# Kernel tuning notes

Hardware: AMD Instinct MI355X
Metric: run time of the kernel (lower is better)

## Reference

```python
import jax, jax.numpy as jnp
import numpy as np

N, D_IN, D_H, D_ATT, C_CLUST, N_CLS = 10000, 1024, 512, 256, 10, 4


def setup_inputs() -> dict:
    key = jax.random.key(0)
    ks = jax.random.split(key, 20)
    s = 0.02
    return {
        "x": jax.random.normal(ks[0], (N, D_IN), dtype=jnp.float32),
        "cluster_id": jax.random.randint(ks[1], (N,), 0, C_CLUST, dtype=jnp.int64),
        # per-cluster phi: Linear(1024->512) + ReLU + Linear(512->512) + ReLU
        "W1": s * jax.random.normal(ks[2], (C_CLUST, D_IN, D_H), dtype=jnp.float32),
        "b1": jnp.zeros((C_CLUST, D_H), dtype=jnp.float32),
        "W2": s * jax.random.normal(ks[3], (C_CLUST, D_H, D_H), dtype=jnp.float32),
        "b2": jnp.zeros((C_CLUST, D_H), dtype=jnp.float32),
        # attention_net fc: Linear(512->512)+ReLU
        "Wfc": s * jax.random.normal(ks[4], (D_H, D_H), dtype=jnp.float32),
        "bfc": jnp.zeros((D_H,), dtype=jnp.float32),
        # Attn_Net_Gated
        "Wa": s * jax.random.normal(ks[5], (D_H, D_ATT), dtype=jnp.float32),
        "ba": jnp.zeros((D_ATT,), dtype=jnp.float32),
        "Wb": s * jax.random.normal(ks[6], (D_H, D_ATT), dtype=jnp.float32),
        "bb": jnp.zeros((D_ATT,), dtype=jnp.float32),
        "Wc": s * jax.random.normal(ks[7], (D_ATT, 1), dtype=jnp.float32),
        "bc": jnp.zeros((1,), dtype=jnp.float32),
        # rho: Linear(512->256)+ReLU
        "Wr": s * jax.random.normal(ks[8], (D_H, D_ATT), dtype=jnp.float32),
        "br": jnp.zeros((D_ATT,), dtype=jnp.float32),
        # classifier: Linear(256->4)
        "Wcls": s * jax.random.normal(ks[9], (D_ATT, N_CLS), dtype=jnp.float32),
        "bcls": jnp.zeros((N_CLS,), dtype=jnp.float32),
    }


def reference(x, cluster_id, W1, b1, W2, b2, Wfc, bfc, Wa, ba, Wb, bb, Wc, bc, Wr, br, Wcls, bcls):
    C = W1.shape[0]
    # dense dispatch: apply every cluster's phi, then masked-mean per cluster
    # (ReLU is per-point elementwise, so masked mean == mean over members)
    h1 = jax.nn.relu(jnp.einsum('nd,cdh->cnh', x, W1) + b1[:, None, :])   # [C,N,512]
    h2 = jax.nn.relu(jnp.einsum('cnh,chk->cnk', h1, W2) + b2[:, None, :]) # [C,N,512]
    mask = (cluster_id[None, :] == jnp.arange(C)[:, None]).astype(h2.dtype)  # [C,N]
    counts = jnp.maximum(mask.sum(axis=1), 1.0)                           # [C]
    pooled = jnp.einsum('cnk,cn->ck', h2, mask) / counts[:, None]         # [C,512]
    # attention_net: fc + gated attention
    h = jax.nn.relu(pooled @ Wfc + bfc)                                   # [C,512]
    gate = jnp.tanh(h @ Wa + ba) * jax.nn.sigmoid(h @ Wb + bb)            # [C,256]
    A = (gate @ Wc + bc)                                                  # [C,1]
    A = jax.nn.softmax(A.T, axis=1)                                       # [1,C]
    h_path = A @ h                                                        # [1,512]
    hr = jax.nn.relu(h_path @ Wr + br)                                    # [1,256]
    logits = (hr[0] @ Wcls + bcls)[None, :]                               # [1,4]
    Y_prob = jax.nn.softmax(logits, axis=1)
    Y_hat = jnp.argmax(logits, axis=1)[:, None]
    return logits, Y_prob, Y_hat
```

## Files before the change

kernel.cpp:

```cpp
#include <hip/hip_runtime.h>
#include <math.h>

#define DIN 1024
#define DH 512
#define DATT 256
#define CNUM 10
#define NCLS 4
#define NH 64
#define NSC 40

typedef __attribute__((ext_vector_type(8))) short bf16x8;
typedef __attribute__((ext_vector_type(4))) float f32x4;
typedef unsigned short ushort_t;
typedef unsigned int uint_t;

__device__ inline ushort_t f2bf(float f) {
    uint_t u = __float_as_uint(f);
    u += 0x7FFF + ((u >> 16) & 1);
    return (ushort_t)(u >> 16);
}

__device__ inline void gl_lds16(const void* g, void* l) {
    __builtin_amdgcn_global_load_lds(
        (const __attribute__((address_space(1))) unsigned int*)g,
        (__attribute__((address_space(3))) unsigned int*)l, 16, 0, 0);
}


__global__ __launch_bounds__(256) void k_hist(
    const int* __restrict__ cid, int n, const float* __restrict__ bc,
    int* __restrict__ counts_part, float* __restrict__ pooled,
    float* __restrict__ a_logit, int* __restrict__ scat_pos)
{
    int bid = blockIdx.x;
    int t = threadIdx.x;

    if (bid < NH) {
        __shared__ int h[CNUM];
        int lane = t & 63;
        if (t < CNUM) h[t] = 0;
        __syncthreads();
        for (int i = bid * 256 + t; i < n; i += NH * 256) {
            int c = cid[i];
            #pragma unroll
            for (int cc = 0; cc < CNUM; cc++) {
                unsigned long long mask = __ballot(c == cc);
                if (mask == 0ull) continue;
                if (lane == (__ffsll(mask) - 1)) atomicAdd(&h[cc], __popcll(mask));
            }
        }
        __syncthreads();
        if (t < CNUM) counts_part[bid * 16 + t] = h[t];
        return;
    }

    for (int i = t; i < CNUM * DH; i += 256) pooled[i] = 0.f;
    if (t < CNUM) a_logit[t] = bc[0];
    if (t < CNUM) scat_pos[t] = 0;
}


__global__ __launch_bounds__(256) void k_scat2(
    const int* __restrict__ cid, int n, const int* __restrict__ counts_part,
    const float* __restrict__ x, const float* __restrict__ W1, const float* __restrict__ W2,
    ushort_t* __restrict__ xb, ushort_t* __restrict__ W1t, ushort_t* __restrict__ W2t,
    int nxb, int nw,
    int* __restrict__ counts, int* __restrict__ offsets, int* __restrict__ tile_off,
    int* __restrict__ scat_pos, int* __restrict__ bucket)
{
    int bid = blockIdx.x;
    int t = threadIdx.x;

    if (bid < NSC) {
        __shared__ int cnts[CNUM], off[CNUM];
        if (t < CNUM) {
            int s = 0;
            #pragma unroll 8
            for (int b = 0; b < NH; b++) s += counts_part[b * 16 + t];
            cnts[t] = s;
        }
        __syncthreads();
        if (t == 0) {
            int a = 0;
            for (int c = 0; c < CNUM; c++) { off[c] = a; a += cnts[c]; }
            if (bid == 0) {
                int aa = 0, tt = 0;
                for (int c = 0; c < CNUM; c++) {
                    offsets[c] = aa; tile_off[c] = tt; counts[c] = cnts[c];
                    aa += cnts[c]; tt += (cnts[c] + 127) >> 7;
                }
                offsets[CNUM] = aa; tile_off[CNUM] = tt;
            }
        }
        __syncthreads();
        int lane = t & 63;
        for (int i = bid * 256 + t; i < n; i += NSC * 256) {
            int c = cid[i];
            #pragma unroll
            for (int cc = 0; cc < CNUM; cc++) {
                unsigned long long mask = __ballot(c == cc);
                if (mask == 0ull) continue;
                int leader = __ffsll(mask) - 1;
                int basep = 0;
                if (lane == leader) basep = atomicAdd(&scat_pos[cc], __popcll(mask));
                basep = __shfl(basep, leader, 64);
                if (c == cc) {
                    int rank = __popcll(mask & ((1ull << lane) - 1ull));
                    bucket[off[cc] + basep + rank] = i;
                }
            }
        }
        return;
    }
    bid -= NSC;

    if (bid < nxb) {
        int row = bid * 2 + (t >> 7);
        if (row >= n) return;
        int col = (t & 127) * 8;
        const float* src = x + (size_t)row * DIN + col;
        float4 v0 = *(const float4*)(src);
        float4 v1 = *(const float4*)(src + 4);
        ushort_t* dst = xb + (size_t)row * DIN + col;
        *(ushort4*)dst = make_ushort4(f2bf(v0.x), f2bf(v0.y), f2bf(v0.z), f2bf(v0.w));
        *(ushort4*)(dst + 4) = make_ushort4(f2bf(v1.x), f2bf(v1.y), f2bf(v1.z), f2bf(v1.w));
        return;
    }
    bid -= nxb;

    if (bid < nw) {
        __shared__ float tile[64][65];
        int z = bid >> 7;
        int kx = (bid & 127) >> 3;
        int ny = bid & 7;
        const float* src; ushort_t* dst; int K;
        if (z < CNUM) { K = DIN; src = W1 + (size_t)z * K * DH; dst = W1t + (size_t)z * DH * K; }
        else          { K = DH;  src = W2 + (size_t)(z - CNUM) * K * DH; dst = W2t + (size_t)(z - CNUM) * DH * K; }
        int k0 = kx * 64;
        if (k0 >= K) return;
        int n0 = ny * 64;
        int rr = t >> 4;
        int cc = (t & 15) * 4;
        #pragma unroll
        for (int i = 0; i < 4; i++) {
            int row = rr + 16 * i;
            float4 v = *(const float4*)(src + (size_t)(k0 + row) * DH + n0 + cc);
            tile[row][cc + 0] = v.x; tile[row][cc + 1] = v.y;
            tile[row][cc + 2] = v.z; tile[row][cc + 3] = v.w;
        }
        __syncthreads();
        #pragma unroll
        for (int i = 0; i < 4; i++) {
            int nrow = rr + 16 * i;
            ushort4 o = make_ushort4(f2bf(tile[cc + 0][nrow]), f2bf(tile[cc + 1][nrow]),
                                     f2bf(tile[cc + 2][nrow]), f2bf(tile[cc + 3][nrow]));
            *(ushort4*)(dst + (size_t)(n0 + nrow) * K + k0 + cc) = o;
        }
    }
}


__device__ inline void gemm_tile(
    const ushort_t* aSrc0, const ushort_t* aSrc1,
    const ushort_t* bSrc0, const ushort_t* bSrc1, int Kd,
    f32x4 acc[4][4], ushort_t As[128][32], ushort_t Bs[128][32])
{
    int t = threadIdx.x;
    int lane = t & 63;
    int w = t >> 6, wr = w >> 1, wc = w & 1;
    int m = lane & 15, quad = lane >> 4;

    int r0 = t >> 2;
    int kc = (t & 3) * 8;

    ushort_t* aDst0 = &As[r0][kc];
    ushort_t* aDst1 = &As[64 + r0][kc];
    ushort_t* bDst0 = &Bs[r0][kc];
    ushort_t* bDst1 = &Bs[64 + r0][kc];

    const ushort_t* aF = &As[64 * wr + m][quad * 8];
    const ushort_t* bF = &Bs[64 * wc + m][quad * 8];

    for (int k0 = 0; k0 < Kd; k0 += 32) {
        __syncthreads();
        gl_lds16(aSrc0 + k0, aDst0);
        gl_lds16(aSrc1 + k0, aDst1);
        gl_lds16(bSrc0 + k0, bDst0);
        gl_lds16(bSrc1 + k0, bDst1);
        __syncthreads();
        bf16x8 a[4], b[4];
        #pragma unroll
        for (int mf = 0; mf < 4; mf++) a[mf] = *(const bf16x8*)(aF + mf * 16 * 32);
        #pragma unroll
        for (int nf = 0; nf < 4; nf++) b[nf] = *(const bf16x8*)(bF + nf * 16 * 32);
        #pragma unroll
        for (int mf = 0; mf < 4; mf++)
            #pragma unroll
            for (int nf = 0; nf < 4; nf++)
                acc[mf][nf] = __builtin_amdgcn_mfma_f32_16x16x32_bf16(a[mf], b[nf], acc[mf][nf], 0, 0, 0);
    }
}

__global__ __launch_bounds__(256, 1) void k_mfma1(
    const ushort_t* __restrict__ xb, const ushort_t* __restrict__ W1t,
    const float* __restrict__ b1, const int* __restrict__ bucket,
    const int* __restrict__ offsets, const int* __restrict__ counts,
    const int* __restrict__ tile_off,
    ushort_t* __restrict__ H1)
{
    __shared__ ushort_t As[128][32];
    __shared__ ushort_t Bs[128][32];
    int tx = blockIdx.y;
    if (tx >= tile_off[CNUM]) return;
    int c = 0;
    while (tx >= tile_off[c + 1]) c++;
    int m0 = (tx - tile_off[c]) * 128;
    int base = offsets[c], cnt = counts[c];
    int tile_n = blockIdx.x * 128;

    int t = threadIdx.x;
    int r0 = t >> 2;
    int kc = (t & 3) * 8;
    int ra0 = m0 + r0;      if (ra0 > cnt - 1) ra0 = cnt - 1; if (ra0 < 0) ra0 = 0;
    int ra1 = m0 + 64 + r0; if (ra1 > cnt - 1) ra1 = cnt - 1; if (ra1 < 0) ra1 = 0;
    const ushort_t* aSrc0 = xb + (size_t)bucket[base + ra0] * DIN + kc;
    const ushort_t* aSrc1 = xb + (size_t)bucket[base + ra1] * DIN + kc;
    const ushort_t* bSrc0 = W1t + ((size_t)c * DH + tile_n + r0) * DIN + kc;
    const ushort_t* bSrc1 = W1t + ((size_t)c * DH + tile_n + 64 + r0) * DIN + kc;

    f32x4 acc[4][4] = {};
    gemm_tile(aSrc0, aSrc1, bSrc0, bSrc1, DIN, acc, As, Bs);

    int lane = t & 63;
    int w = t >> 6, wr = w >> 1, wc = w & 1;
    int m = lane & 15, quad = lane >> 4;
    int col0 = tile_n + 64 * wc;
    #pragma unroll
    for (int nf = 0; nf < 4; nf++) {
        int col = col0 + 16 * nf + m;
        float bv = b1[c * DH + col];
        #pragma unroll
        for (int mf = 0; mf < 4; mf++) {
            int rowb = m0 + 64 * wr + 16 * mf + quad * 4;
            #pragma unroll
            for (int r = 0; r < 4; r++) {
                int row = rowb + r;
                if (row < cnt)
                    H1[(size_t)(base + row) * DH + col] = f2bf(fmaxf(acc[mf][nf][r] + bv, 0.f));
            }
        }
    }
}

__global__ __launch_bounds__(256, 1) void k_mfma2(
    const ushort_t* __restrict__ H1, const ushort_t* __restrict__ W2t,
    const float* __restrict__ b2,
    const int* __restrict__ offsets, const int* __restrict__ counts,
    const int* __restrict__ tile_off,
    float* __restrict__ pooled)
{
    __shared__ ushort_t As[128][32];
    __shared__ ushort_t Bs[128][32];
    int tx = blockIdx.y;
    if (tx >= tile_off[CNUM]) return;
    int c = 0;
    while (tx >= tile_off[c + 1]) c++;
    int m0 = (tx - tile_off[c]) * 128;
    int base = offsets[c], cnt = counts[c];
    int tile_n = blockIdx.x * 128;

    int t = threadIdx.x;
    int r0 = t >> 2;
    int kc = (t & 3) * 8;
    int ra0 = m0 + r0;      if (ra0 > cnt - 1) ra0 = cnt - 1; if (ra0 < 0) ra0 = 0;
    int ra1 = m0 + 64 + r0; if (ra1 > cnt - 1) ra1 = cnt - 1; if (ra1 < 0) ra1 = 0;
    const ushort_t* aSrc0 = H1 + (size_t)(base + ra0) * DH + kc;
    const ushort_t* aSrc1 = H1 + (size_t)(base + ra1) * DH + kc;
    const ushort_t* bSrc0 = W2t + ((size_t)c * DH + tile_n + r0) * DH + kc;
    const ushort_t* bSrc1 = W2t + ((size_t)c * DH + tile_n + 64 + r0) * DH + kc;

    f32x4 acc[4][4] = {};
    gemm_tile(aSrc0, aSrc1, bSrc0, bSrc1, DH, acc, As, Bs);

    int lane = t & 63;
    int w = t >> 6, wr = w >> 1, wc = w & 1;
    int m = lane & 15, quad = lane >> 4;
    int col0 = tile_n + 64 * wc;
    #pragma unroll
    for (int nf = 0; nf < 4; nf++) {
        int col = col0 + 16 * nf + m;
        float bv = b2[c * DH + col];
        float s = 0.f;
        #pragma unroll
        for (int mf = 0; mf < 4; mf++) {
            int rowb = m0 + 64 * wr + 16 * mf + quad * 4;
            #pragma unroll
            for (int r = 0; r < 4; r++) {
                int row = rowb + r;
                if (row < cnt) s += fmaxf(acc[mf][nf][r] + bv, 0.f);
            }
        }
        s += __shfl_xor(s, 16);
        s += __shfl_xor(s, 32);
        if (quad == 0) atomicAdd(&pooled[c * DH + col], s);
    }
}


__global__ __launch_bounds__(256) void k_fc2(
    const float* __restrict__ pooled, const int* __restrict__ counts,
    const float* __restrict__ Wfc, const float* __restrict__ bfc,
    float* __restrict__ hfc)
{
    int c = blockIdx.x;
    int c0 = blockIdx.y * 64;
    __shared__ float ps[DH];
    __shared__ float red[4][64];
    int t = threadIdx.x;
    float cnt = fmaxf((float)counts[c], 1.f);
    ps[t] = pooled[c * DH + t] / cnt;
    ps[t + 256] = pooled[c * DH + t + 256] / cnt;
    __syncthreads();
    int col = c0 + (t & 63);
    int ks = t >> 6;
    float acc = 0.f;
    #pragma unroll 8
    for (int k = ks * 128; k < ks * 128 + 128; k++)
        acc = fmaf(ps[k], Wfc[(size_t)k * DH + col], acc);
    red[ks][t & 63] = acc;
    __syncthreads();
    if (t < 64) {
        float v = red[0][t] + red[1][t] + red[2][t] + red[3][t] + bfc[c0 + t];
        hfc[c * DH + c0 + t] = fmaxf(v, 0.f);
    }
}

__global__ __launch_bounds__(256) void k_gate2(
    const float* __restrict__ hfc,
    const float* __restrict__ Wa, const float* __restrict__ ba,
    const float* __restrict__ Wb, const float* __restrict__ bb,
    const float* __restrict__ Wc,
    float* __restrict__ a_logit)
{
    int c = blockIdx.x;
    int d0 = blockIdx.y * 64;
    __shared__ float hf[DH];
    __shared__ float ra[4][64], rb[4][64];
    int t = threadIdx.x;
    hf[t] = hfc[c * DH + t];
    hf[t + 256] = hfc[c * DH + t + 256];
    __syncthreads();
    int d = d0 + (t & 63);
    int ks = t >> 6;
    float ga = 0.f, gb = 0.f;
    #pragma unroll 8
    for (int k = ks * 128; k < ks * 128 + 128; k++) {
        float h = hf[k];
        ga = fmaf(h, Wa[(size_t)k * DATT + d], ga);
        gb = fmaf(h, Wb[(size_t)k * DATT + d], gb);
    }
    ra[ks][t & 63] = ga;
    rb[ks][t & 63] = gb;
    __syncthreads();
    if (t < 64) {
        float sa = ra[0][t] + ra[1][t] + ra[2][t] + ra[3][t] + ba[d0 + t];
        float sb = rb[0][t] + rb[1][t] + rb[2][t] + rb[3][t] + bb[d0 + t];
        float g = tanhf(sa) * (1.f / (1.f + expf(-sb)));
        float p = g * Wc[d0 + t];
        #pragma unroll
        for (int off = 32; off >= 1; off >>= 1) p += __shfl_down(p, off, 64);
        if (t == 0) atomicAdd(&a_logit[c], p);
    }
}

__global__ __launch_bounds__(1024) void k_final(
    const float* __restrict__ hfc, const float* __restrict__ a_logit,
    const float* __restrict__ Wr, const float* __restrict__ br,
    const float* __restrict__ Wcls, const float* __restrict__ bcls,
    float* __restrict__ out)
{
    int t = threadIdx.x;
    __shared__ float hp[DH];
    __shared__ float r1[4][DATT];
    __shared__ float hr[DATT];
    __shared__ float wred[4][NCLS];

    float al[CNUM];
    float m = -1e30f;
    #pragma unroll
    for (int c = 0; c < CNUM; c++) { al[c] = a_logit[c]; m = fmaxf(m, al[c]); }
    float s = 0.f;
    #pragma unroll
    for (int c = 0; c < CNUM; c++) { al[c] = expf(al[c] - m); s += al[c]; }
    float inv = 1.f / s;

    if (t < DH) {
        float v = 0.f;
        #pragma unroll
        for (int c = 0; c < CNUM; c++) v = fmaf(al[c] * inv, hfc[c * DH + t], v);
        hp[t] = v;
    }
    __syncthreads();

    int d = t & 255;
    int ks = t >> 8;
    float acc = 0.f;
    #pragma unroll 8
    for (int k = ks * 128; k < ks * 128 + 128; k++)
        acc = fmaf(hp[k], Wr[(size_t)k * DATT + d], acc);
    r1[ks][d] = acc;
    __syncthreads();
    if (t < DATT)
        hr[t] = fmaxf(r1[0][t] + r1[1][t] + r1[2][t] + r1[3][t] + br[t], 0.f);
    __syncthreads();

    if (t < 256) {
        float h = hr[t];
        #pragma unroll
        for (int cls = 0; cls < NCLS; cls++) {
            float p = h * Wcls[(size_t)t * NCLS + cls];
            #pragma unroll
            for (int off = 32; off >= 1; off >>= 1) p += __shfl_down(p, off, 64);
            if ((t & 63) == 0) wred[t >> 6][cls] = p;
        }
    }
    __syncthreads();
    if (t == 0) {
        float lg[NCLS];
        #pragma unroll
        for (int cls = 0; cls < NCLS; cls++)
            lg[cls] = bcls[cls] + wred[0][cls] + wred[1][cls] + wred[2][cls] + wred[3][cls];
        float mm = lg[0];
        #pragma unroll
        for (int i = 1; i < NCLS; i++) mm = fmaxf(mm, lg[i]);
        float ss = 0.f, pr[NCLS];
        #pragma unroll
        for (int i = 0; i < NCLS; i++) { pr[i] = expf(lg[i] - mm); ss += pr[i]; }
        int am = 0; float best = lg[0];
        #pragma unroll
        for (int i = 1; i < NCLS; i++) if (lg[i] > best) { best = lg[i]; am = i; }
        #pragma unroll
        for (int i = 0; i < NCLS; i++) out[i] = lg[i];
        #pragma unroll
        for (int i = 0; i < NCLS; i++) out[4 + i] = pr[i] / ss;
        out[8] = (float)am;
    }
}


#define MT 64
#define NT 128
#define KT 32

__global__ __launch_bounds__(256) void k_gemm1(
    const float* __restrict__ x, const float* __restrict__ W1, const float* __restrict__ b1,
    const int* __restrict__ bucket, const int* __restrict__ offsets, const int* __restrict__ counts,
    float* __restrict__ H1)
{
    int c = blockIdx.z;
    int cnt = counts[c];
    int m0 = blockIdx.x * MT;
    if (m0 >= cnt) return;
    int rows = min(MT, cnt - m0);
    int n0 = blockIdx.y * NT;
    int base = offsets[c];

    __shared__ float As[KT][MT + 4];
    __shared__ float Bs[KT][NT];

    int t = threadIdx.x;
    int tr = t >> 4;
    int tc = t & 15;
    int lr = t >> 2;
    int lk = (t & 3) * 8;
    const float* xrow = nullptr;
    if (lr < rows) xrow = x + (size_t)bucket[base + m0 + lr] * DIN;

    float acc[4][8];
    #pragma unroll
    for (int i = 0; i < 4; i++)
        #pragma unroll
        for (int j = 0; j < 8; j++) acc[i][j] = 0.f;

    const float* Wp = W1 + (size_t)c * DIN * DH + n0;

    for (int k0 = 0; k0 < DIN; k0 += KT) {
        __syncthreads();
        if (xrow) {
            float4 v0 = *(const float4*)(xrow + k0 + lk);
            float4 v1 = *(const float4*)(xrow + k0 + lk + 4);
            As[lk + 0][lr] = v0.x; As[lk + 1][lr] = v0.y;
            As[lk + 2][lr] = v0.z; As[lk + 3][lr] = v0.w;
            As[lk + 4][lr] = v1.x; As[lk + 5][lr] = v1.y;
            As[lk + 6][lr] = v1.z; As[lk + 7][lr] = v1.w;
        } else {
            #pragma unroll
            for (int i = 0; i < 8; i++) As[lk + i][lr] = 0.f;
        }
        #pragma unroll
        for (int i = 0; i < 4; i++) {
            int idx = i * 256 + t;
            int kk = idx >> 5;
            int cv = idx & 31;
            *(float4*)&Bs[kk][cv * 4] = *(const float4*)(Wp + (size_t)(k0 + kk) * DH + cv * 4);
        }
        __syncthreads();
        #pragma unroll
        for (int k = 0; k < KT; k++) {
            float4 av  = *(const float4*)&As[k][4 * tr];
            float4 bv0 = *(const float4*)&Bs[k][4 * tc];
            float4 bv1 = *(const float4*)&Bs[k][64 + 4 * tc];
            float a[4] = {av.x, av.y, av.z, av.w};
            float b[8] = {bv0.x, bv0.y, bv0.z, bv0.w, bv1.x, bv1.y, bv1.z, bv1.w};
            #pragma unroll
            for (int i = 0; i < 4; i++)
                #pragma unroll
                for (int j = 0; j < 8; j++)
                    acc[i][j] = fmaf(a[i], b[j], acc[i][j]);
        }
    }

    #pragma unroll
    for (int i = 0; i < 4; i++) {
        int r = 4 * tr + i;
        if (r < rows) {
            size_t grow = (size_t)(base + m0 + r) * DH;
            #pragma unroll
            for (int j = 0; j < 8; j++) {
                int cidx = (j < 4) ? (4 * tc + j) : (64 + 4 * tc + (j - 4));
                int col = n0 + cidx;
                float v = acc[i][j] + b1[c * DH + col];
                H1[grow + col] = fmaxf(v, 0.f);
            }
        }
    }
}

__global__ __launch_bounds__(256) void k_gemm2(
    const float* __restrict__ H1, const float* __restrict__ W2, const float* __restrict__ b2,
    const int* __restrict__ offsets, const int* __restrict__ counts,
    float* __restrict__ pooled)
{
    int c = blockIdx.z;
    int cnt = counts[c];
    int m0 = blockIdx.x * MT;
    if (m0 >= cnt) return;
    int rows = min(MT, cnt - m0);
    int n0 = blockIdx.y * NT;
    int base = offsets[c];

    __shared__ float As[KT][MT + 4];
    __shared__ float Bs[KT][NT];
    __shared__ float red[16][NT];

    int t = threadIdx.x;
    int tr = t >> 4;
    int tc = t & 15;
    int lr = t >> 2;
    int lk = (t & 3) * 8;
    const float* arow = (lr < rows) ? (H1 + (size_t)(base + m0 + lr) * DH) : nullptr;

    float acc[4][8];
    #pragma unroll
    for (int i = 0; i < 4; i++)
        #pragma unroll
        for (int j = 0; j < 8; j++) acc[i][j] = 0.f;

    const float* Wp = W2 + (size_t)c * DH * DH + n0;

    for (int k0 = 0; k0 < DH; k0 += KT) {
        __syncthreads();
        if (arow) {
            float4 v0 = *(const float4*)(arow + k0 + lk);
            float4 v1 = *(const float4*)(arow + k0 + lk + 4);
            As[lk + 0][lr] = v0.x; As[lk + 1][lr] = v0.y;
            As[lk + 2][lr] = v0.z; As[lk + 3][lr] = v0.w;
            As[lk + 4][lr] = v1.x; As[lk + 5][lr] = v1.y;
            As[lk + 6][lr] = v1.z; As[lk + 7][lr] = v1.w;
        } else {
            #pragma unroll
            for (int i = 0; i < 8; i++) As[lk + i][lr] = 0.f;
        }
        #pragma unroll
        for (int i = 0; i < 4; i++) {
            int idx = i * 256 + t;
            int kk = idx >> 5;
            int cv = idx & 31;
            *(float4*)&Bs[kk][cv * 4] = *(const float4*)(Wp + (size_t)(k0 + kk) * DH + cv * 4);
        }
        __syncthreads();
        #pragma unroll
        for (int k = 0; k < KT; k++) {
            float4 av  = *(const float4*)&As[k][4 * tr];
            float4 bv0 = *(const float4*)&Bs[k][4 * tc];
            float4 bv1 = *(const float4*)&Bs[k][64 + 4 * tc];
            float a[4] = {av.x, av.y, av.z, av.w};
            float b[8] = {bv0.x, bv0.y, bv0.z, bv0.w, bv1.x, bv1.y, bv1.z, bv1.w};
            #pragma unroll
            for (int i = 0; i < 4; i++)
                #pragma unroll
                for (int j = 0; j < 8; j++)
                    acc[i][j] = fmaf(a[i], b[j], acc[i][j]);
        }
    }

    __syncthreads();
    #pragma unroll
    for (int j = 0; j < 8; j++) {
        int cidx = (j < 4) ? (4 * tc + j) : (64 + 4 * tc + (j - 4));
        float bias = b2[c * DH + n0 + cidx];
        float s = 0.f;
        #pragma unroll
        for (int i = 0; i < 4; i++) {
            if (4 * tr + i < rows) s += fmaxf(acc[i][j] + bias, 0.f);
        }
        red[tr][cidx] = s;
    }
    __syncthreads();
    if (t < NT) {
        float s = 0.f;
        #pragma unroll
        for (int r = 0; r < 16; r++) s += red[r][t];
        atomicAdd(&pooled[c * DH + n0 + t], s);
    }
}


extern "C" void kernel_launch(void* const* d_in, const int* in_sizes, int n_in,
                              void* d_out, int out_size, void* d_ws, size_t ws_size,
                              hipStream_t stream) {
    (void)n_in; (void)out_size;
    const float* x    = (const float*)d_in[0];
    const int*   cid  = (const int*)d_in[1];
    const float* W1   = (const float*)d_in[2];
    const float* b1   = (const float*)d_in[3];
    const float* W2   = (const float*)d_in[4];
    const float* b2   = (const float*)d_in[5];
    const float* Wfc  = (const float*)d_in[6];
    const float* bfc  = (const float*)d_in[7];
    const float* Wa   = (const float*)d_in[8];
    const float* ba   = (const float*)d_in[9];
    const float* Wb   = (const float*)d_in[10];
    const float* bb   = (const float*)d_in[11];
    const float* Wc   = (const float*)d_in[12];
    const float* bc   = (const float*)d_in[13];
    const float* Wr   = (const float*)d_in[14];
    const float* br   = (const float*)d_in[15];
    const float* Wcls = (const float*)d_in[16];
    const float* bcls = (const float*)d_in[17];
    float* out = (float*)d_out;
    float* ws  = (float*)d_ws;

    int n = in_sizes[1];

    float* pooled     = ws + 0;
    int*   counts     = (int*)(ws + 5120);
    int*   offsets    = (int*)(ws + 5136);
    int*   tile_off   = (int*)(ws + 5152);
    float* a_logit    = ws + 5168;
    int*   scat_pos   = (int*)(ws + 5184);
    float* hfc        = ws + 5200;
    int*   counts_part= (int*)(ws + 10320);
    int*   bucket     = (int*)(ws + 11344);

    size_t big0 = (((size_t)(11344 + n) * 4) + 255) & ~(size_t)255;
    size_t w1t_bytes = (size_t)CNUM * DH * DIN * 2;
    size_t w2t_bytes = (size_t)CNUM * DH * DH * 2;
    size_t h1_bytes  = (size_t)n * DH * 2;
    size_t xb_bytes  = (size_t)n * DIN * 2;
    size_t need = big0 + w1t_bytes + w2t_bytes + h1_bytes + xb_bytes;

    ushort_t* W1t = (ushort_t*)((char*)d_ws + big0);
    ushort_t* W2t = (ushort_t*)((char*)d_ws + big0 + w1t_bytes);
    ushort_t* H1  = (ushort_t*)((char*)d_ws + big0 + w1t_bytes + w2t_bytes);
    ushort_t* xb  = (ushort_t*)((char*)d_ws + big0 + w1t_bytes + w2t_bytes + h1_bytes);

    int fast = (ws_size >= need) ? 1 : 0;
    int nxb = fast ? (n + 1) / 2 : 0;
    int nw  = fast ? 128 * 2 * CNUM : 0;

    k_hist<<<NH + 1, 256, 0, stream>>>(cid, n, bc, counts_part, pooled, a_logit, scat_pos);
    k_scat2<<<NSC + nxb + nw, 256, 0, stream>>>(
        cid, n, counts_part, x, W1, W2, xb, W1t, W2t, nxb, nw,
        counts, offsets, tile_off, scat_pos, bucket);

    if (fast) {
        int maxt = n / 128 + CNUM;
        k_mfma1<<<dim3(4, maxt), 256, 0, stream>>>(xb, W1t, b1, bucket, offsets, counts, tile_off, H1);
        k_mfma2<<<dim3(4, maxt), 256, 0, stream>>>(H1, W2t, b2, offsets, counts, tile_off, pooled);
    } else {
        float* H1f = ws + ((11344 + n + 31) & ~31);
        dim3 gg((n + MT - 1) / MT, DH / NT, CNUM);
        k_gemm1<<<gg, 256, 0, stream>>>(x, W1, b1, bucket, offsets, counts, H1f);
        k_gemm2<<<gg, 256, 0, stream>>>(H1f, W2, b2, offsets, counts, pooled);
    }

    k_fc2<<<dim3(CNUM, 8), 256, 0, stream>>>(pooled, counts, Wfc, bfc, hfc);
    k_gate2<<<dim3(CNUM, 4), 256, 0, stream>>>(hfc, Wa, ba, Wb, bb, Wc, a_logit);
    k_final<<<1, 1024, 0, stream>>>(hfc, a_logit, Wr, br, Wcls, bcls, out);
}
```

Baseline: 230.4 us.

## Drop histogram pass, use per-cluster buckets and double-buffered swizzled MFMA GEMMs

Removes the separate histogram kernel by giving each cluster a fixed bucket region of size n, so the scatter atomics alone produce the counts; pooled and scat_pos are zeroed with a memset. The MFMA GEMMs move to K=64 tiles with double-buffered LDS, XOR-swizzled layout, explicit waitcnt and barrier scheduling, and an XCD-aware flat tile ordering. This is meant to cut a kernel launch and a serial dependency and to overlap global-to-LDS loads with MFMA work. In exchange the bucket and H1 buffers grow to CNUM*n, which raises workspace size. The change also uses more LDS per block, which may lower occupancy.

```diff
diff --git a/kernel.cpp b/kernel.cpp
--- a/kernel.cpp
+++ b/kernel.cpp
@@ -27,72 +27,23 @@
 }
 
 
-__global__ __launch_bounds__(256) void k_hist(
+__global__ __launch_bounds__(256) void k_prep(
     const int* __restrict__ cid, int n, const float* __restrict__ bc,
-    int* __restrict__ counts_part, float* __restrict__ pooled,
-    float* __restrict__ a_logit, int* __restrict__ scat_pos)
-{
-    int bid = blockIdx.x;
-    int t = threadIdx.x;
-
-    if (bid < NH) {
-        __shared__ int h[CNUM];
-        int lane = t & 63;
-        if (t < CNUM) h[t] = 0;
-        __syncthreads();
-        for (int i = bid * 256 + t; i < n; i += NH * 256) {
-            int c = cid[i];
-            #pragma unroll
-            for (int cc = 0; cc < CNUM; cc++) {
-                unsigned long long mask = __ballot(c == cc);
-                if (mask == 0ull) continue;
-                if (lane == (__ffsll(mask) - 1)) atomicAdd(&h[cc], __popcll(mask));
-            }
-        }
-        __syncthreads();
-        if (t < CNUM) counts_part[bid * 16 + t] = h[t];
-        return;
-    }
-
-    for (int i = t; i < CNUM * DH; i += 256) pooled[i] = 0.f;
-    if (t < CNUM) a_logit[t] = bc[0];
-    if (t < CNUM) scat_pos[t] = 0;
-}
-
-
-__global__ __launch_bounds__(256) void k_scat2(
-    const int* __restrict__ cid, int n, const int* __restrict__ counts_part,
     const float* __restrict__ x, const float* __restrict__ W1, const float* __restrict__ W2,
     ushort_t* __restrict__ xb, ushort_t* __restrict__ W1t, ushort_t* __restrict__ W2t,
     int nxb, int nw,
-    int* __restrict__ counts, int* __restrict__ offsets, int* __restrict__ tile_off,
-    int* __restrict__ scat_pos, int* __restrict__ bucket)
+    float* __restrict__ a_logit, int* __restrict__ scat_pos, int* __restrict__ bucket)
 {
     int bid = blockIdx.x;
     int t = threadIdx.x;
 
+    if (bid == 0) {
+        if (t < CNUM) a_logit[t] = bc[0];
+        return;
+    }
+    bid -= 1;
+
     if (bid < NSC) {
-        __shared__ int cnts[CNUM], off[CNUM];
-        if (t < CNUM) {
-            int s = 0;
-            #pragma unroll 8
-            for (int b = 0; b < NH; b++) s += counts_part[b * 16 + t];
-            cnts[t] = s;
-        }
-        __syncthreads();
-        if (t == 0) {
-            int a = 0;
-            for (int c = 0; c < CNUM; c++) { off[c] = a; a += cnts[c]; }
-            if (bid == 0) {
-                int aa = 0, tt = 0;
-                for (int c = 0; c < CNUM; c++) {
-                    offsets[c] = aa; tile_off[c] = tt; counts[c] = cnts[c];
-                    aa += cnts[c]; tt += (cnts[c] + 127) >> 7;
-                }
-                offsets[CNUM] = aa; tile_off[CNUM] = tt;
-            }
-        }
-        __syncthreads();
         int lane = t & 63;
         for (int i = bid * 256 + t; i < n; i += NSC * 256) {
             int c = cid[i];
@@ -106,7 +57,7 @@
                 basep = __shfl(basep, leader, 64);
                 if (c == cc) {
                     int rank = __popcll(mask & ((1ull << lane) - 1ull));
-                    bucket[off[cc] + basep + rank] = i;
+                    bucket[cc * n + basep + rank] = i;
                 }
             }
         }
@@ -115,15 +66,16 @@
     bid -= NSC;
 
     if (bid < nxb) {
-        int row = bid * 2 + (t >> 7);
+        int row = bid * 4 + (t >> 6);
         if (row >= n) return;
-        int col = (t & 127) * 8;
+        int col = (t & 63) * 16;
         const float* src = x + (size_t)row * DIN + col;
-        float4 v0 = *(const float4*)(src);
-        float4 v1 = *(const float4*)(src + 4);
         ushort_t* dst = xb + (size_t)row * DIN + col;
-        *(ushort4*)dst = make_ushort4(f2bf(v0.x), f2bf(v0.y), f2bf(v0.z), f2bf(v0.w));
-        *(ushort4*)(dst + 4) = make_ushort4(f2bf(v1.x), f2bf(v1.y), f2bf(v1.z), f2bf(v1.w));
+        #pragma unroll
+        for (int j = 0; j < 4; j++) {
+            float4 v = *(const float4*)(src + 4 * j);
+            *(ushort4*)(dst + 4 * j) = make_ushort4(f2bf(v.x), f2bf(v.y), f2bf(v.z), f2bf(v.w));
+        }
         return;
     }
     bid -= nxb;
@@ -160,76 +112,132 @@
 }
 
 
-__device__ inline void gemm_tile(
-    const ushort_t* aSrc0, const ushort_t* aSrc1,
-    const ushort_t* bSrc0, const ushort_t* bSrc1, int Kd,
-    f32x4 acc[4][4], ushort_t As[128][32], ushort_t Bs[128][32])
+__device__ inline void stage8(
+    const ushort_t* a0, const ushort_t* a1, const ushort_t* a2, const ushort_t* a3,
+    const ushort_t* b0, const ushort_t* b1, const ushort_t* b2, const ushort_t* b3,
+    int ko, ushort_t* As, ushort_t* Bs, int t)
+{
+    gl_lds16(a0 + ko, As + 0 * 2048 + t * 8);
+    gl_lds16(a1 + ko, As + 1 * 2048 + t * 8);
+    gl_lds16(a2 + ko, As + 2 * 2048 + t * 8);
+    gl_lds16(a3 + ko, As + 3 * 2048 + t * 8);
+    gl_lds16(b0 + ko, Bs + 0 * 2048 + t * 8);
+    gl_lds16(b1 + ko, Bs + 1 * 2048 + t * 8);
+    gl_lds16(b2 + ko, Bs + 2 * 2048 + t * 8);
+    gl_lds16(b3 + ko, Bs + 3 * 2048 + t * 8);
+}
+
+__device__ inline void mfma_tile(const ushort_t* As, const ushort_t* Bs,
+                                 f32x4 (&acc)[4][4], int wr, int wc, int m, int quad)
+{
+    bf16x8 a[2][4], b[2][4];
+    #pragma unroll
+    for (int ks = 0; ks < 2; ks++) {
+        int chunk = ((ks * 4 + quad) ^ (m & 7)) * 8;
+        #pragma unroll
+        for (int mf = 0; mf < 4; mf++)
+            a[ks][mf] = *(const bf16x8*)(As + (64 * wr + 16 * mf + m) * 64 + chunk);
+        #pragma unroll
+        for (int nf = 0; nf < 4; nf++)
+            b[ks][nf] = *(const bf16x8*)(Bs + (64 * wc + 16 * nf + m) * 64 + chunk);
+    }
+    asm volatile("s_waitcnt lgkmcnt(0)" ::: "memory");
+    __builtin_amdgcn_sched_barrier(0);
+    __builtin_amdgcn_s_barrier();
+    __builtin_amdgcn_sched_barrier(0);
+    #pragma unroll
+    for (int ks = 0; ks < 2; ks++)
+        #pragma unroll
+        for (int mf = 0; mf < 4; mf++)
+            #pragma unroll
+            for (int nf = 0; nf < 4; nf++)
+                acc[mf][nf] = __builtin_amdgcn_mfma_f32_16x16x32_bf16(a[ks][mf], b[ks][nf], acc[mf][nf], 0, 0, 0);
+}
+
+__device__ inline void gemm_loop(
+    const ushort_t* a0, const ushort_t* a1, const ushort_t* a2, const ushort_t* a3,
+    const ushort_t* b0, const ushort_t* b1, const ushort_t* b2, const ushort_t* b3,
+    int KT, f32x4 (&acc)[4][4], ushort_t* As, ushort_t* Bs)
 {
     int t = threadIdx.x;
     int lane = t & 63;
     int w = t >> 6, wr = w >> 1, wc = w & 1;
     int m = lane & 15, quad = lane >> 4;
 
-    int r0 = t >> 2;
-    int kc = (t & 3) * 8;
-
-    ushort_t* aDst0 = &As[r0][kc];
-    ushort_t* aDst1 = &As[64 + r0][kc];
-    ushort_t* bDst0 = &Bs[r0][kc];
-    ushort_t* bDst1 = &Bs[64 + r0][kc];
-
-    const ushort_t* aF = &As[64 * wr + m][quad * 8];
-    const ushort_t* bF = &Bs[64 * wc + m][quad * 8];
-
-    for (int k0 = 0; k0 < Kd; k0 += 32) {
-        __syncthreads();
-        gl_lds16(aSrc0 + k0, aDst0);
-        gl_lds16(aSrc1 + k0, aDst1);
-        gl_lds16(bSrc0 + k0, bDst0);
-        gl_lds16(bSrc1 + k0, bDst1);
-        __syncthreads();
-        bf16x8 a[4], b[4];
-        #pragma unroll
-        for (int mf = 0; mf < 4; mf++) a[mf] = *(const bf16x8*)(aF + mf * 16 * 32);
-        #pragma unroll
-        for (int nf = 0; nf < 4; nf++) b[nf] = *(const bf16x8*)(bF + nf * 16 * 32);
-        #pragma unroll
-        for (int mf = 0; mf < 4; mf++)
-            #pragma unroll
-            for (int nf = 0; nf < 4; nf++)
-                acc[mf][nf] = __builtin_amdgcn_mfma_f32_16x16x32_bf16(a[mf], b[nf], acc[mf][nf], 0, 0, 0);
-    }
-}
-
-__global__ __launch_bounds__(256, 1) void k_mfma1(
+    stage8(a0, a1, a2, a3, b0, b1, b2, b3, 0, As, Bs, t);
+    for (int kt = 0; kt < KT; kt += 2) {
+        stage8(a0, a1, a2, a3, b0, b1, b2, b3, (kt + 1) * 64, As + 8192, Bs + 8192, t);
+        asm volatile("s_waitcnt vmcnt(8)" ::: "memory");
+        __builtin_amdgcn_sched_barrier(0);
+        __builtin_amdgcn_s_barrier();
+        __builtin_amdgcn_sched_barrier(0);
+        mfma_tile(As, Bs, acc, wr, wc, m, quad);
+
+        if (kt + 2 < KT) {
+            stage8(a0, a1, a2, a3, b0, b1, b2, b3, (kt + 2) * 64, As, Bs, t);
+            asm volatile("s_waitcnt vmcnt(8)" ::: "memory");
+        } else {
+            asm volatile("s_waitcnt vmcnt(0)" ::: "memory");
+        }
+        __builtin_amdgcn_sched_barrier(0);
+        __builtin_amdgcn_s_barrier();
+        __builtin_amdgcn_sched_barrier(0);
+        mfma_tile(As + 8192, Bs + 8192, acc, wr, wc, m, quad);
+    }
+}
+
+__device__ inline int tile_decode(int bid, int MAXT, const int* counts,
+                                  int& c, int& m0, int& tile_n)
+{
+    int mt, nt;
+    if ((MAXT & 7) == 0) {
+        int mtpx = MAXT >> 3;
+        int xcd = bid & 7, j = bid >> 3;
+        nt = j / mtpx;
+        mt = xcd * mtpx + (j - nt * mtpx);
+    } else { mt = bid >> 2; nt = bid & 3; }
+
+    int rem = mt;
+    c = 0;
+    #pragma unroll
+    for (int cc = 0; cc < CNUM; cc++) {
+        int tc = (counts[cc] + 127) >> 7;
+        if (rem < tc) { c = cc; m0 = rem * 128; tile_n = nt * 128; return 1; }
+        rem -= tc;
+    }
+    return 0;
+}
+
+__global__ __launch_bounds__(256) void k_g1(
     const ushort_t* __restrict__ xb, const ushort_t* __restrict__ W1t,
     const float* __restrict__ b1, const int* __restrict__ bucket,
-    const int* __restrict__ offsets, const int* __restrict__ counts,
-    const int* __restrict__ tile_off,
+    const int* __restrict__ counts, int n, int MAXT,
     ushort_t* __restrict__ H1)
 {
-    __shared__ ushort_t As[128][32];
-    __shared__ ushort_t Bs[128][32];
-    int tx = blockIdx.y;
-    if (tx >= tile_off[CNUM]) return;
-    int c = 0;
-    while (tx >= tile_off[c + 1]) c++;
-    int m0 = (tx - tile_off[c]) * 128;
-    int base = offsets[c], cnt = counts[c];
-    int tile_n = blockIdx.x * 128;
-
-    int t = threadIdx.x;
-    int r0 = t >> 2;
-    int kc = (t & 3) * 8;
-    int ra0 = m0 + r0;      if (ra0 > cnt - 1) ra0 = cnt - 1; if (ra0 < 0) ra0 = 0;
-    int ra1 = m0 + 64 + r0; if (ra1 > cnt - 1) ra1 = cnt - 1; if (ra1 < 0) ra1 = 0;
-    const ushort_t* aSrc0 = xb + (size_t)bucket[base + ra0] * DIN + kc;
-    const ushort_t* aSrc1 = xb + (size_t)bucket[base + ra1] * DIN + kc;
-    const ushort_t* bSrc0 = W1t + ((size_t)c * DH + tile_n + r0) * DIN + kc;
-    const ushort_t* bSrc1 = W1t + ((size_t)c * DH + tile_n + 64 + r0) * DIN + kc;
+    __shared__ ushort_t As[2][128][64];
+    __shared__ ushort_t Bs[2][128][64];
+
+    int c, m0, tile_n;
+    if (!tile_decode(blockIdx.x, MAXT, counts, c, m0, tile_n)) return;
+    int cnt = counts[c];
+
+    int t = threadIdx.x;
+    int rr = t >> 3;
+    int swz = ((t & 7) ^ (rr & 7)) * 8;
+
+    const ushort_t* aP[4];
+    const ushort_t* bP[4];
+    #pragma unroll
+    for (int s = 0; s < 4; s++) {
+        int ra = m0 + s * 32 + rr;
+        if (ra > cnt - 1) ra = cnt - 1;
+        aP[s] = xb + (size_t)bucket[c * n + ra] * DIN + swz;
+        bP[s] = W1t + ((size_t)c * DH + tile_n + s * 32 + rr) * DIN + swz;
+    }
 
     f32x4 acc[4][4] = {};
-    gemm_tile(aSrc0, aSrc1, bSrc0, bSrc1, DIN, acc, As, Bs);
+    gemm_loop(aP[0], aP[1], aP[2], aP[3], bP[0], bP[1], bP[2], bP[3],
+              DIN / 64, acc, &As[0][0][0], &Bs[0][0][0]);
 
     int lane = t & 63;
     int w = t >> 6, wr = w >> 1, wc = w & 1;
@@ -246,41 +254,41 @@
             for (int r = 0; r < 4; r++) {
                 int row = rowb + r;
                 if (row < cnt)
-                    H1[(size_t)(base + row) * DH + col] = f2bf(fmaxf(acc[mf][nf][r] + bv, 0.f));
+                    H1[((size_t)c * n + row) * DH + col] = f2bf(fmaxf(acc[mf][nf][r] + bv, 0.f));
             }
         }
     }
 }
 
-__global__ __launch_bounds__(256, 1) void k_mfma2(
+__global__ __launch_bounds__(256) void k_g2(
     const ushort_t* __restrict__ H1, const ushort_t* __restrict__ W2t,
-    const float* __restrict__ b2,
-    const int* __restrict__ offsets, const int* __restrict__ counts,
-    const int* __restrict__ tile_off,
+    const float* __restrict__ b2, const int* __restrict__ counts, int n, int MAXT,
     float* __restrict__ pooled)
 {
-    __shared__ ushort_t As[128][32];
-    __shared__ ushort_t Bs[128][32];
-    int tx = blockIdx.y;
-    if (tx >= tile_off[CNUM]) return;
-    int c = 0;
-    while (tx >= tile_off[c + 1]) c++;
-    int m0 = (tx - tile_off[c]) * 128;
-    int base = offsets[c], cnt = counts[c];
-    int tile_n = blockIdx.x * 128;
-
-    int t = threadIdx.x;
-    int r0 = t >> 2;
-    int kc = (t & 3) * 8;
-    int ra0 = m0 + r0;      if (ra0 > cnt - 1) ra0 = cnt - 1; if (ra0 < 0) ra0 = 0;
-    int ra1 = m0 + 64 + r0; if (ra1 > cnt - 1) ra1 = cnt - 1; if (ra1 < 0) ra1 = 0;
-    const ushort_t* aSrc0 = H1 + (size_t)(base + ra0) * DH + kc;
-    const ushort_t* aSrc1 = H1 + (size_t)(base + ra1) * DH + kc;
-    const ushort_t* bSrc0 = W2t + ((size_t)c * DH + tile_n + r0) * DH + kc;
-    const ushort_t* bSrc1 = W2t + ((size_t)c * DH + tile_n + 64 + r0) * DH + kc;
+    __shared__ ushort_t As[2][128][64];
+    __shared__ ushort_t Bs[2][128][64];
+
+    int c, m0, tile_n;
+    if (!tile_decode(blockIdx.x, MAXT, counts, c, m0, tile_n)) return;
+    int cnt = counts[c];
+
+    int t = threadIdx.x;
+    int rr = t >> 3;
+    int swz = ((t & 7) ^ (rr & 7)) * 8;
+
+    const ushort_t* aP[4];
+    const ushort_t* bP[4];
+    #pragma unroll
+    for (int s = 0; s < 4; s++) {
+        int ra = m0 + s * 32 + rr;
+        if (ra > cnt - 1) ra = cnt - 1;
+        aP[s] = H1 + ((size_t)c * n + ra) * DH + swz;
+        bP[s] = W2t + ((size_t)c * DH + tile_n + s * 32 + rr) * DH + swz;
+    }
 
     f32x4 acc[4][4] = {};
-    gemm_tile(aSrc0, aSrc1, bSrc0, bSrc1, DH, acc, As, Bs);
+    gemm_loop(aP[0], aP[1], aP[2], aP[3], bP[0], bP[1], bP[2], bP[3],
+              DH / 64, acc, &As[0][0][0], &Bs[0][0][0]);
 
     int lane = t & 63;
     int w = t >> 6, wr = w >> 1, wc = w & 1;
@@ -447,6 +455,82 @@
     }
 }
 
+
+__global__ __launch_bounds__(256) void k_hist(
+    const int* __restrict__ cid, int n, const float* __restrict__ bc,
+    int* __restrict__ counts_part, float* __restrict__ pooled,
+    float* __restrict__ a_logit, int* __restrict__ scat_pos)
+{
+    int bid = blockIdx.x;
+    int t = threadIdx.x;
+
+    if (bid < NH) {
+        __shared__ int h[CNUM];
+        int lane = t & 63;
+        if (t < CNUM) h[t] = 0;
+        __syncthreads();
+        for (int i = bid * 256 + t; i < n; i += NH * 256) {
+            int c = cid[i];
+            #pragma unroll
+            for (int cc = 0; cc < CNUM; cc++) {
+                unsigned long long mask = __ballot(c == cc);
+                if (mask == 0ull) continue;
+                if (lane == (__ffsll(mask) - 1)) atomicAdd(&h[cc], __popcll(mask));
+            }
+        }
+        __syncthreads();
+        if (t < CNUM) counts_part[bid * 16 + t] = h[t];
+        return;
+    }
+
+    for (int i = t; i < CNUM * DH; i += 256) pooled[i] = 0.f;
+    if (t < CNUM) a_logit[t] = bc[0];
+    if (t < CNUM) scat_pos[t] = 0;
+}
+
+__global__ __launch_bounds__(256) void k_scat_fb(
+    const int* __restrict__ cid, int n, const int* __restrict__ counts_part,
+    int* __restrict__ counts, int* __restrict__ offsets,
+    int* __restrict__ scat_pos, int* __restrict__ bucket)
+{
+    int bid = blockIdx.x;
+    int t = threadIdx.x;
+    __shared__ int cnts[CNUM], off[CNUM];
+    if (t < CNUM) {
+        int s = 0;
+        #pragma unroll 8
+        for (int b = 0; b < NH; b++) s += counts_part[b * 16 + t];
+        cnts[t] = s;
+    }
+    __syncthreads();
+    if (t == 0) {
+        int a = 0;
+        for (int c = 0; c < CNUM; c++) { off[c] = a; a += cnts[c]; }
+        if (bid == 0) {
+            int aa = 0;
+            for (int c = 0; c < CNUM; c++) { offsets[c] = aa; counts[c] = cnts[c]; aa += cnts[c]; }
+            offsets[CNUM] = aa;
+        }
+    }
+    __syncthreads();
+    int lane = t & 63;
+    for (int i = bid * 256 + t; i < n; i += NSC * 256) {
+        int c = cid[i];
+        #pragma unroll
+        for (int cc = 0; cc < CNUM; cc++) {
+            unsigned long long mask = __ballot(c == cc);
+            if (mask == 0ull) continue;
+            int leader = __ffsll(mask) - 1;
+            int basep = 0;
+            if (lane == leader) basep = atomicAdd(&scat_pos[cc], __popcll(mask));
+            basep = __shfl(basep, leader, 64);
+            if (c == cc) {
+                int rank = __popcll(mask & ((1ull << lane) - 1ull));
+                bucket[off[cc] + basep + rank] = i;
+            }
+        }
+    }
+}
 
 #define MT 64
 #define NT 128
@@ -653,49 +737,57 @@
 
     int n = in_sizes[1];
 
-    float* pooled     = ws + 0;
-    int*   counts     = (int*)(ws + 5120);
-    int*   offsets    = (int*)(ws + 5136);
-    int*   tile_off   = (int*)(ws + 5152);
-    float* a_logit    = ws + 5168;
-    int*   scat_pos   = (int*)(ws + 5184);
-    float* hfc        = ws + 5200;
-    int*   counts_part= (int*)(ws + 10320);
-    int*   bucket     = (int*)(ws + 11344);
-
-    size_t big0 = (((size_t)(11344 + n) * 4) + 255) & ~(size_t)255;
+    float* pooled   = ws;
+    int*   scat_pos = (int*)(ws + 5120);
+    float* a_logit  = ws + 5136;
+    float* hfc      = ws + 5152;
+    int*   bucket   = (int*)(ws + 10272);
+
+    size_t big0 = (((size_t)(10272 + (size_t)CNUM * n) * 4) + 255) & ~(size_t)255;
     size_t w1t_bytes = (size_t)CNUM * DH * DIN * 2;
     size_t w2t_bytes = (size_t)CNUM * DH * DH * 2;
-    size_t h1_bytes  = (size_t)n * DH * 2;
+    size_t h1_bytes  = (size_t)CNUM * n * DH * 2;
     size_t xb_bytes  = (size_t)n * DIN * 2;
     size_t need = big0 + w1t_bytes + w2t_bytes + h1_bytes + xb_bytes;
 
-    ushort_t* W1t = (ushort_t*)((char*)d_ws + big0);
-    ushort_t* W2t = (ushort_t*)((char*)d_ws + big0 + w1t_bytes);
-    ushort_t* H1  = (ushort_t*)((char*)d_ws + big0 + w1t_bytes + w2t_bytes);
-    ushort_t* xb  = (ushort_t*)((char*)d_ws + big0 + w1t_bytes + w2t_bytes + h1_bytes);
-
-    int fast = (ws_size >= need) ? 1 : 0;
-    int nxb = fast ? (n + 1) / 2 : 0;
-    int nw  = fast ? 128 * 2 * CNUM : 0;
-
-    k_hist<<<NH + 1, 256, 0, stream>>>(cid, n, bc, counts_part, pooled, a_logit, scat_pos);
-    k_scat2<<<NSC + nxb + nw, 256, 0, stream>>>(
-        cid, n, counts_part, x, W1, W2, xb, W1t, W2t, nxb, nw,
-        counts, offsets, tile_off, scat_pos, bucket);
-
-    if (fast) {
-        int maxt = n / 128 + CNUM;
-        k_mfma1<<<dim3(4, maxt), 256, 0, stream>>>(xb, W1t, b1, bucket, offsets, counts, tile_off, H1);
-        k_mfma2<<<dim3(4, maxt), 256, 0, stream>>>(H1, W2t, b2, offsets, counts, tile_off, pooled);
+    if (ws_size >= need) {
+        ushort_t* W1t = (ushort_t*)((char*)d_ws + big0);
+        ushort_t* W2t = (ushort_t*)((char*)d_ws + big0 + w1t_bytes);
+        ushort_t* H1  = (ushort_t*)((char*)d_ws + big0 + w1t_bytes + w2t_bytes);
+        ushort_t* xb  = (ushort_t*)((char*)d_ws + big0 + w1t_bytes + w2t_bytes + h1_bytes);
+
+        int nxb = (n + 3) / 4;
+        int nw  = 128 * 2 * CNUM;
+        int MAXT = ((n / 128) + CNUM + 1) & ~1;
+
+        hipMemsetAsync(ws, 0, 5136 * 4, stream);
+        k_prep<<<1 + NSC + nxb + nw, 256, 0, stream>>>(
+            cid, n, bc, x, W1, W2, xb, W1t, W2t, nxb, nw, a_logit, scat_pos, bucket);
+        k_g1<<<4 * MAXT, 256, 0, stream>>>(xb, W1t, b1, bucket, scat_pos, n, MAXT, H1);
+        k_g2<<<4 * MAXT, 256, 0, stream>>>(H1, W2t, b2, scat_pos, n, MAXT, pooled);
+        k_fc2<<<dim3(CNUM, 8), 256, 0, stream>>>(pooled, scat_pos, Wfc, bfc, hfc);
+        k_gate2<<<dim3(CNUM, 4), 256, 0, stream>>>(hfc, Wa, ba, Wb, bb, Wc, a_logit);
+        k_final<<<1, 1024, 0, stream>>>(hfc, a_logit, Wr, br, Wcls, bcls, out);
     } else {
+        float* pooledF     = ws + 0;
+        int*   countsF     = (int*)(ws + 5120);
+        int*   offsetsF    = (int*)(ws + 5136);
+        float* a_logitF    = ws + 5168;
+        int*   scat_posF   = (int*)(ws + 5184);
+        float* hfcF        = ws + 5200;
+        int*   counts_part = (int*)(ws + 10320);
+        int*   bucketF     = (int*)(ws + 11344);
+
+        k_hist<<<NH + 1, 256, 0, stream>>>(cid, n, bc, counts_part, pooledF, a_logitF, scat_posF);
+        k_scat_fb<<<NSC, 256, 0, stream>>>(cid, n, counts_part, countsF, offsetsF, scat_posF, bucketF);
+
         float* H1f = ws + ((11344 + n + 31) & ~31);
         dim3 gg((n + MT - 1) / MT, DH / NT, CNUM);
-        k_gemm1<<<gg, 256, 0, stream>>>(x, W1, b1, bucket, offsets, counts, H1f);
-        k_gemm2<<<gg, 256, 0, stream>>>(H1f, W2, b2, offsets, counts, pooled);
-    }
-
-    k_fc2<<<dim3(CNUM, 8), 256, 0, stream>>>(pooled, counts, Wfc, bfc, hfc);
-    k_gate2<<<dim3(CNUM, 4), 256, 0, stream>>>(hfc, Wa, ba, Wb, bb, Wc, a_logit);
-    k_final<<<1, 1024, 0, stream>>>(hfc, a_logit, Wr, br, Wcls, bcls, out);
-}
+        k_gemm1<<<gg, 256, 0, stream>>>(x, W1, b1, bucketF, offsetsF, countsF, H1f);
+        k_gemm2<<<gg, 256, 0, stream>>>(H1f, W2, b2, offsetsF, countsF, pooledF);
+
+        k_fc2<<<dim3(CNUM, 8), 256, 0, stream>>>(pooledF, countsF, Wfc, bfc, hfcF);
+        k_gate2<<<dim3(CNUM, 4), 256, 0, stream>>>(hfcF, Wa, ba, Wb, bb, Wc, a_logitF);
+        k_final<<<1, 1024, 0, stream>>>(hfcF, a_logitF, Wr, br, Wcls, bcls, out);
+    }
+}
```

Measured after the change: 218.7 us. 5.1% less time.
